# Performance work log

Measured on AMD Instinct MI355X. Metric: run time of the kernel, lower is better.

The kernel has to match this reference:

```python
import jax, jax.numpy as jnp
import numpy as np

B, N, FA, FP, C = 64, 64, 75, 14, 128


def _mlp2(x, W0, b0, W1, b1):
    # two lazy-Linear + ReLU sub-layers (n_sub_layer=2)
    h = jax.nn.relu(x @ W0 + b0)
    return jax.nn.relu(h @ W1 + b1)


def setup_inputs() -> dict:
    key = jax.random.key(0)
    ks = jax.random.split(key, 32)
    w = lambda k, s: jax.random.normal(k, s, jnp.float32) * 0.05
    inp = {
        "atom_x": jax.random.normal(ks[0], (B, N, FA), jnp.float32),
        "pair_x": jax.random.normal(ks[1], (B, N * N, FP), jnp.float32),
        # atom_to_atom: FA -> C -> C
        "a2a_W0": w(ks[2], (FA, C)), "a2a_b0": w(ks[3], (C,)),
        "a2a_W1": w(ks[4], (C, C)), "a2a_b1": w(ks[5], (C,)),
        # pair_to_atom: FP -> C -> C
        "p2a_W0": w(ks[6], (FP, C)), "p2a_b0": w(ks[7], (C,)),
        "p2a_W1": w(ks[8], (C, C)), "p2a_b1": w(ks[9], (C,)),
        # atom_layer: 2C -> C -> C
        "al_W0": w(ks[10], (2 * C, C)), "al_b0": w(ks[11], (C,)),
        "al_W1": w(ks[12], (C, C)), "al_b1": w(ks[13], (C,)),
        # atom_to_pair (weights shared across both orderings): 2FA -> C -> C
        "a2p_W0": w(ks[14], (2 * FA, C)), "a2p_b0": w(ks[15], (C,)),
        "a2p_W1": w(ks[16], (C, C)), "a2p_b1": w(ks[17], (C,)),
        # pair_to_pair: FP -> C -> C
        "p2p_W0": w(ks[18], (FP, C)), "p2p_b0": w(ks[19], (C,)),
        "p2p_W1": w(ks[20], (C, C)), "p2p_b1": w(ks[21], (C,)),
        # pair_layer: 2C -> C -> C
        "pl_W0": w(ks[22], (2 * C, C)), "pl_b0": w(ks[23], (C,)),
        "pl_W1": w(ks[24], (C, C)), "pl_b1": w(ks[25], (C,)),
    }
    return inp


def reference(atom_x, pair_x,
              a2a_W0, a2a_b0, a2a_W1, a2a_b1,
              p2a_W0, p2a_b0, p2a_W1, p2a_b1,
              al_W0, al_b0, al_W1, al_b1,
              a2p_W0, a2p_b0, a2p_W1, a2p_b1,
              p2p_W0, p2p_b0, p2p_W1, p2p_b1,
              pl_W0, pl_b0, pl_W1, pl_b1):
    b, n, fa = atom_x.shape
    # --- atom branch ---
    a0 = _mlp2(atom_x, a2a_W0, a2a_b0, a2a_W1, a2a_b1)            # [B,N,C]
    a1 = _mlp2(pair_x, p2a_W0, p2a_b0, p2a_W1, p2a_b1)            # [B,N*N,C]
    a1 = a1.reshape(b, n, n, -1).sum(axis=2)                      # PairToAtom sum
    a = jnp.concatenate([a0, a1], axis=-1)                        # [B,N,2C]
    next_atom = jax.nn.relu(_mlp2(a, al_W0, al_b0, al_W1, al_b1))  # extra relu per forward
    # --- pair branch ---
    rep = jnp.broadcast_to(atom_x[:, None, :, :], (b, n, n, fa))  # atom_repeat
    til = jnp.broadcast_to(atom_x[:, :, None, :], (b, n, n, fa))  # atom_tile
    pr0 = jnp.concatenate([til, rep], axis=-1).reshape(b, n * n, 2 * fa)
    pr1 = jnp.concatenate([rep, til], axis=-1).reshape(b, n * n, 2 * fa)
    p0 = (_mlp2(pr0, a2p_W0, a2p_b0, a2p_W1, a2p_b1)
          + _mlp2(pr1, a2p_W0, a2p_b0, a2p_W1, a2p_b1))            # [B,N*N,C]
    p1 = _mlp2(pair_x, p2p_W0, p2p_b0, p2p_W1, p2p_b1)            # [B,N*N,C]
    p = jnp.concatenate([p0, p1], axis=-1)                        # [B,N*N,2C]
    next_pair = jax.nn.relu(_mlp2(p, pl_W0, pl_b0, pl_W1, pl_b1))
    return (next_atom, next_pair)
```

## Files before the change

### kernel.cpp

```cpp
#include <hip/hip_runtime.h>
#include <hip/hip_bf16.h>

typedef unsigned short u16;
typedef unsigned int u32;
typedef __attribute__((ext_vector_type(8))) __bf16 bf16x8;
typedef __attribute__((ext_vector_type(4))) float f32x4;

#define B_ 64
#define N_ 64
#define FA_ 75
#define FP_ 14
#define C_ 128

__device__ float g_A0[4096 * 128];
__device__ float g_A1[4096 * 128];
__device__ float g_TB[4096 * 256];
__device__ u16   g_Wf[208896];
__device__ int   g_isbf;

#define OFF_AA0   0
#define OFF_AA1   12288
#define OFF_APT   28672
#define OFF_APB   40960
#define OFF_PA0   53248
#define OFF_PA1   57344
#define OFF_AL0   73728
#define OFF_AL1   106496
#define OFF_AP1   122880
#define OFF_PP0   139264
#define OFF_PP1   143360
#define OFF_PL0T  159744
#define OFF_PL0B  176128
#define OFF_PL1   192512

__device__ __forceinline__ float bf2f(u16 a) {
    union { u32 u; float f; } v; v.u = ((u32)a) << 16; return v.f;
}
__device__ __forceinline__ u16 f2bf(float f) {
    union { float f; u32 u; } v; v.f = f;
    u32 r = v.u + 0x7fffu + ((v.u >> 16) & 1u);
    return (u16)(r >> 16);
}
__device__ __forceinline__ u16 ldw(const void* p, size_t i, bool isbf) {
    if (isbf) return ((const u16*)p)[i];
    return f2bf(((const float*)p)[i]);
}
__device__ __forceinline__ float ldf(const void* p, size_t i, bool isbf) {
    if (isbf) return bf2f(((const u16*)p)[i]);
    return ((const float*)p)[i];
}

__global__ void detect_k(const void* __restrict__ atom) {
    if (threadIdx.x == 0) {
        const u32* a = (const u32*)atom;
        int sane = 0;
        for (int w = 0; w < 64; ++w) {
            u32 ex = (a[w] >> 7) & 0xffu;
            sane += (ex >= 113u && ex <= 133u) ? 1 : 0;
        }
        g_isbf = (sane >= 32) ? 1 : 0;
    }
}

__global__ __launch_bounds__(256) void prep_w(
    const void* aaW0, const void* aaW1, const void* apW0,
    const void* paW0, const void* paW1, const void* alW0, const void* alW1,
    const void* apW1, const void* ppW0, const void* ppW1,
    const void* plW0, const void* plW1) {
    const void* srcs[14] = {aaW0, aaW1, apW0, apW0, paW0, paW1, alW0, alW1,
                            apW1, ppW0, ppW1, plW0, plW0, plW1};
    const int Ktab[14]  = {75, 128, 75, 75, 14, 128, 256, 128, 128, 14, 128, 128, 128, 128};
    const int KStab[14] = {3, 4, 3, 3, 1, 4, 8, 4, 4, 1, 4, 4, 4, 4};
    const int rofft[14] = {0, 0, 0, 75, 0, 0, 0, 0, 0, 0, 0, 0, 128, 0};
    const int baset[14] = {OFF_AA0, OFF_AA1, OFF_APT, OFF_APB, OFF_PA0, OFF_PA1,
                           OFF_AL0, OFF_AL1, OFF_AP1, OFF_PP0, OFF_PP1,
                           OFF_PL0T, OFF_PL0B, OFF_PL1};
    int gid = blockIdx.x * 256 + threadIdx.x;
    int j = 0, s = gid;
    while (j < 14 && s >= KStab[j] * 512) { s -= KStab[j] * 512; ++j; }
    if (j >= 14) return;
    const bool isbf = g_isbf != 0;
    int lane = s & 63, rest = s >> 6;
    int ks = rest % KStab[j], mt = rest / KStab[j];
    int m = mt * 16 + (lane & 15), q = lane >> 4;
    union { u16 h[8]; uint4 u4; } pk;
#pragma unroll
    for (int jj = 0; jj < 8; ++jj) {
        int k = ks * 32 + q * 8 + jj;
        pk.h[jj] = (k < Ktab[j]) ? ldw(srcs[j], (size_t)(rofft[j] + k) * 128 + m, isbf) : (u16)0;
    }
    *(uint4*)&g_Wf[(size_t)baset[j] + (size_t)s * 8] = pk.u4;
}

template<int KS, int NT>
__device__ __forceinline__ void gemm2(const u16* __restrict__ wf,
                                      const u16* __restrict__ bF,
                                      int mt0, int lane, f32x4 (&acc)[2][NT]) {
#pragma unroll
    for (int ks = 0; ks < KS; ++ks) {
        bf16x8 a0 = *(const bf16x8*)(wf + (((mt0    ) * KS + ks) * 64 + lane) * 8);
        bf16x8 a1 = *(const bf16x8*)(wf + (((mt0 + 1) * KS + ks) * 64 + lane) * 8);
#pragma unroll
        for (int nt = 0; nt < NT; ++nt) {
            bf16x8 b = *(const bf16x8*)(bF + ((nt * KS + ks) * 64 + lane) * 8);
            acc[0][nt] = __builtin_amdgcn_mfma_f32_16x16x32_bf16(a0, b, acc[0][nt], 0, 0, 0);
            acc[1][nt] = __builtin_amdgcn_mfma_f32_16x16x32_bf16(a1, b, acc[1][nt], 0, 0, 0);
        }
    }
}

__device__ __forceinline__ void frag_store(u16* dstF, int KSd, int nt, int mt, int lane, f32x4 v) {
    int c = lane & 15, quad = lane >> 4;
    int lp = c + 16 * ((2 * mt + (quad >> 1)) & 3);
    int ks = mt >> 1;
    u16* p = dstF + (((nt * KSd + ks) * 64 + lp) * 8 + (quad & 1) * 4);
    union { u16 h[4]; uint2 u; } pk;
    pk.h[0] = f2bf(v[0]); pk.h[1] = f2bf(v[1]); pk.h[2] = f2bf(v[2]); pk.h[3] = f2bf(v[3]);
    *(uint2*)p = pk.u;
}

__device__ __forceinline__ void store_out4(void* outp, size_t elem, f32x4 v, bool isbf) {
    if (isbf) {
        union { u16 h[4]; uint2 u; } pk;
        pk.h[0] = f2bf(v[0]); pk.h[1] = f2bf(v[1]); pk.h[2] = f2bf(v[2]); pk.h[3] = f2bf(v[3]);
        *(uint2*)((u16*)outp + elem) = pk.u;
    } else {
        *(f32x4*)((float*)outp + elem) = v;
    }
}

#define EPI_RELU_STORE(ACC, SB, DST, NTN) do {                                   \
    int quad_ = lane >> 4;                                                       \
    _Pragma("unroll") for (int ii = 0; ii < 2; ++ii) {                           \
        int mt_ = mt0 + ii;                                                      \
        f32x4 bb_ = *(const f32x4*)&SB[mt_ * 16 + quad_ * 4];                    \
        _Pragma("unroll") for (int nt_ = 0; nt_ < NTN; ++nt_) {                  \
            f32x4 v_;                                                            \
            _Pragma("unroll") for (int r_ = 0; r_ < 4; ++r_) {                   \
                float x_ = ACC[ii][nt_][r_] + bb_[r_];                           \
                v_[r_] = x_ > 0.f ? x_ : 0.f;                                    \
            }                                                                    \
            frag_store(DST, 4, nt_, mt_, lane, v_);                              \
        }                                                                        \
    }                                                                            \
} while (0)

__global__ __launch_bounds__(256) void atom_pre(
    const void* __restrict__ atom,
    const void* __restrict__ aaB0, const void* __restrict__ aaB1) {
    __shared__ __align__(16) u16 sXF[4 * 3 * 64 * 8];
    __shared__ __align__(16) u16 sHF[4 * 4 * 64 * 8];
    __shared__ __align__(16) float sB0[128], sB1[128];
    const bool isbf = g_isbf != 0;
    const int t = threadIdx.x, lane = t & 63, w = t >> 6;
    const int b = blockIdx.x;
    if (t < 128) { sB0[t] = ldf(aaB0, t, isbf); sB1[t] = ldf(aaB1, t, isbf); }
    for (int s = t; s < 4 * 3 * 64; s += 256) {
        int lane_s = s & 63, rest = s >> 6;
        int ks = rest % 3, nt = rest / 3;
        int n = nt * 16 + (lane_s & 15), q = lane_s >> 4;
        union { u16 h[8]; uint4 u4; } pk;
#pragma unroll
        for (int j = 0; j < 8; ++j) {
            int k = ks * 32 + q * 8 + j;
            pk.h[j] = (k < FA_) ? ldw(atom, (size_t)(b * 64 + n) * FA_ + k, isbf) : (u16)0;
        }
        *(uint4*)&sXF[s * 8] = pk.u4;
    }
    __syncthreads();
    const int mt0 = 2 * w;
    {
        f32x4 acc[2][4];
#pragma unroll
        for (int ii = 0; ii < 2; ++ii)
#pragma unroll
            for (int nt = 0; nt < 4; ++nt) acc[ii][nt] = (f32x4){0.f, 0.f, 0.f, 0.f};
        gemm2<3, 4>(g_Wf + OFF_AA0, sXF, mt0, lane, acc);
        EPI_RELU_STORE(acc, sB0, sHF, 4);
    }
    __syncthreads();
    {
        f32x4 acc[2][4];
#pragma unroll
        for (int ii = 0; ii < 2; ++ii)
#pragma unroll
            for (int nt = 0; nt < 4; ++nt) acc[ii][nt] = (f32x4){0.f, 0.f, 0.f, 0.f};
        gemm2<4, 4>(g_Wf + OFF_AA1, sHF, mt0, lane, acc);
        int c = lane & 15, quad = lane >> 4;
#pragma unroll
        for (int ii = 0; ii < 2; ++ii) {
            int mt = mt0 + ii;
            f32x4 bb = *(const f32x4*)&sB1[mt * 16 + quad * 4];
#pragma unroll
            for (int nt = 0; nt < 4; ++nt) {
                f32x4 v;
#pragma unroll
                for (int r = 0; r < 4; ++r) { float x = acc[ii][nt][r] + bb[r]; v[r] = x > 0.f ? x : 0.f; }
                *(f32x4*)&g_A0[(size_t)(b * 64 + nt * 16 + c) * 128 + mt * 16 + quad * 4] = v;
            }
        }
    }
    {
        f32x4 accT[2][4], accB[2][4];
#pragma unroll
        for (int ii = 0; ii < 2; ++ii)
#pragma unroll
            for (int nt = 0; nt < 4; ++nt) { accT[ii][nt] = (f32x4){0.f,0.f,0.f,0.f}; accB[ii][nt] = (f32x4){0.f,0.f,0.f,0.f}; }
        gemm2<3, 4>(g_Wf + OFF_APT, sXF, mt0, lane, accT);
        gemm2<3, 4>(g_Wf + OFF_APB, sXF, mt0, lane, accB);
        int c = lane & 15, quad = lane >> 4;
#pragma unroll
        for (int ii = 0; ii < 2; ++ii) {
            int mt = mt0 + ii;
#pragma unroll
            for (int nt = 0; nt < 4; ++nt) {
                size_t row = (size_t)(b * 64 + nt * 16 + c);
                *(f32x4*)&g_TB[row * 256 + mt * 16 + quad * 4] = accT[ii][nt];
                *(f32x4*)&g_TB[row * 256 + 128 + mt * 16 + quad * 4] = accB[ii][nt];
            }
        }
    }
}

__global__ __launch_bounds__(256) void p2a_sum(
    const void* __restrict__ pairx,
    const void* __restrict__ paB0, const void* __restrict__ paB1) {
    __shared__ __align__(16) u16 sPF[4 * 1 * 64 * 8];
    __shared__ __align__(16) u16 sHF[4 * 4 * 64 * 8];
    __shared__ __align__(16) float sB0[128], sB1[128];
    const bool isbf = g_isbf != 0;
    const int t = threadIdx.x, lane = t & 63, w = t >> 6;
    const int bx = blockIdx.x;
    const size_t rbase = (size_t)bx * 64;
    if (t < 128) { sB0[t] = ldf(paB0, t, isbf); sB1[t] = ldf(paB1, t, isbf); }
    if (t < 256) {
        int s = t;
        int lane_s = s & 63, nt = s >> 6;
        int n = nt * 16 + (lane_s & 15), q = lane_s >> 4;
        union { u16 h[8]; uint4 u4; } pk;
#pragma unroll
        for (int j = 0; j < 8; ++j) {
            int k = q * 8 + j;
            pk.h[j] = (k < FP_) ? ldw(pairx, (rbase + n) * FP_ + k, isbf) : (u16)0;
        }
        *(uint4*)&sPF[s * 8] = pk.u4;
    }
    __syncthreads();
    const int mt0 = 2 * w;
    {
        f32x4 acc[2][4];
#pragma unroll
        for (int ii = 0; ii < 2; ++ii)
#pragma unroll
            for (int nt = 0; nt < 4; ++nt) acc[ii][nt] = (f32x4){0.f, 0.f, 0.f, 0.f};
        gemm2<1, 4>(g_Wf + OFF_PA0, sPF, mt0, lane, acc);
        EPI_RELU_STORE(acc, sB0, sHF, 4);
    }
    __syncthreads();
    {
        f32x4 acc[2][4];
#pragma unroll
        for (int ii = 0; ii < 2; ++ii)
#pragma unroll
            for (int nt = 0; nt < 4; ++nt) acc[ii][nt] = (f32x4){0.f, 0.f, 0.f, 0.f};
        gemm2<4, 4>(g_Wf + OFF_PA1, sHF, mt0, lane, acc);
        int quad = lane >> 4;
#pragma unroll
        for (int ii = 0; ii < 2; ++ii) {
            int mt = mt0 + ii;
            f32x4 bb = *(const f32x4*)&sB1[mt * 16 + quad * 4];
            f32x4 ssum = (f32x4){0.f, 0.f, 0.f, 0.f};
#pragma unroll
            for (int nt = 0; nt < 4; ++nt)
#pragma unroll
                for (int r = 0; r < 4; ++r) {
                    float x = acc[ii][nt][r] + bb[r];
                    ssum[r] += (x > 0.f ? x : 0.f);
                }
#pragma unroll
            for (int m = 1; m < 16; m <<= 1)
#pragma unroll
                for (int r = 0; r < 4; ++r) ssum[r] += __shfl_xor(ssum[r], m, 64);
            if ((lane & 15) == 0)
                *(f32x4*)&g_A1[(size_t)bx * 128 + mt * 16 + quad * 4] = ssum;
        }
    }
}

__global__ __launch_bounds__(256) void atom_layer(
    const void* __restrict__ alB0, const void* __restrict__ alB1,
    void* __restrict__ out) {
    __shared__ __align__(16) u16 sXF[2 * 8 * 64 * 8];
    __shared__ __align__(16) u16 sHF[2 * 4 * 64 * 8];
    __shared__ __align__(16) float sB0[128], sB1[128];
    const bool isbf = g_isbf != 0;
    const int t = threadIdx.x, lane = t & 63, w = t >> 6;
    const int r0g = blockIdx.x * 32;
    if (t < 128) { sB0[t] = ldf(alB0, t, isbf); sB1[t] = ldf(alB1, t, isbf); }
    for (int s = t; s < 2 * 8 * 64; s += 256) {
        int lane_s = s & 63, rest = s >> 6;
        int ks = rest % 8, nt = rest / 8;
        int n = nt * 16 + (lane_s & 15), q = lane_s >> 4;
        union { u16 h[8]; uint4 u4; } pk;
#pragma unroll
        for (int j = 0; j < 8; ++j) {
            int k = ks * 32 + q * 8 + j;
            float v = (k < 128) ? g_A0[(size_t)(r0g + n) * 128 + k]
                                : g_A1[(size_t)(r0g + n) * 128 + (k - 128)];
            pk.h[j] = f2bf(v);
        }
        *(uint4*)&sXF[s * 8] = pk.u4;
    }
    __syncthreads();
    const int mt0 = 2 * w;
    {
        f32x4 acc[2][2];
#pragma unroll
        for (int ii = 0; ii < 2; ++ii)
#pragma unroll
            for (int nt = 0; nt < 2; ++nt) acc[ii][nt] = (f32x4){0.f, 0.f, 0.f, 0.f};
        gemm2<8, 2>(g_Wf + OFF_AL0, sXF, mt0, lane, acc);
        EPI_RELU_STORE(acc, sB0, sHF, 2);
    }
    __syncthreads();
    {
        f32x4 acc[2][2];
#pragma unroll
        for (int ii = 0; ii < 2; ++ii)
#pragma unroll
            for (int nt = 0; nt < 2; ++nt) acc[ii][nt] = (f32x4){0.f, 0.f, 0.f, 0.f};
        gemm2<4, 2>(g_Wf + OFF_AL1, sHF, mt0, lane, acc);
        int c = lane & 15, quad = lane >> 4;
#pragma unroll
        for (int ii = 0; ii < 2; ++ii) {
            int mt = mt0 + ii;
            f32x4 bb = *(const f32x4*)&sB1[mt * 16 + quad * 4];
#pragma unroll
            for (int nt = 0; nt < 2; ++nt) {
                f32x4 v;
#pragma unroll
                for (int r = 0; r < 4; ++r) { float x = acc[ii][nt][r] + bb[r]; v[r] = x > 0.f ? x : 0.f; }
                store_out4(out, (size_t)(r0g + nt * 16 + c) * 128 + mt * 16 + quad * 4, v, isbf);
            }
        }
    }
}

__global__ __launch_bounds__(256) void pair_fused(
    const void* __restrict__ pairx,
    const void* __restrict__ apB0, const void* __restrict__ apB1,
    const void* __restrict__ ppB0, const void* __restrict__ ppB1,
    const void* __restrict__ plB0, const void* __restrict__ plB1,
    void* __restrict__ out) {
    __shared__ __align__(16) u16 sPrF[2 * 1 * 64 * 8];
    __shared__ __align__(16) u16 sH0F[2 * 4 * 64 * 8];
    __shared__ __align__(16) u16 sH1F[2 * 4 * 64 * 8];
    __shared__ __align__(16) u16 sP0F[2 * 4 * 64 * 8];
    __shared__ __align__(16) u16 sHpF[2 * 4 * 64 * 8];
    __shared__ __align__(16) float sBap0[128], sBap1[128], sBpp0[128],
                                   sBpp1[128], sBpl0[128], sBpl1[128];
    const bool isbf = g_isbf != 0;
    const int t = threadIdx.x, lane = t & 63, w = t >> 6;
    const int bx = blockIdx.x;
    const int b = bx >> 7, i = (bx >> 1) & 63, half = bx & 1;
    const int jbase = half * 32, trow = b * 64;
    const size_t prow0 = (size_t)b * 4096 + i * 64 + jbase;

    if (t < 128) {
        sBap0[t] = ldf(apB0, t, isbf); sBap1[t] = ldf(apB1, t, isbf);
        sBpp0[t] = ldf(ppB0, t, isbf); sBpp1[t] = ldf(ppB1, t, isbf);
        sBpl0[t] = ldf(plB0, t, isbf); sBpl1[t] = ldf(plB1, t, isbf);
    }
    if (t < 128) {
        int s = t;
        int lane_s = s & 63, nt = s >> 6;
        int n = nt * 16 + (lane_s & 15), q = lane_s >> 4;
        union { u16 h[8]; uint4 u4; } pk;
#pragma unroll
        for (int j = 0; j < 8; ++j) {
            int k = q * 8 + j;
            pk.h[j] = (k < FP_) ? ldw(pairx, (prow0 + n) * FP_ + k, isbf) : (u16)0;
        }
        *(uint4*)&sPrF[s * 8] = pk.u4;
    }
    __syncthreads();
    for (int sid = t; sid < 1024; sid += 256) {
        int bufid = sid >> 9;
        int s = sid & 511;
        int lane_s = s & 63, rest = s >> 6;
        int ks = rest & 3, nt = rest >> 2;
        int n = nt * 16 + (lane_s & 15), q = lane_s >> 4;
        int k0 = ks * 32 + q * 8;
        const float* Ti = &g_TB[(size_t)(trow + i) * 256];
        const float* Bj = &g_TB[(size_t)(trow + jbase + n) * 256];
        union { u16 h[8]; uint4 u4; } pk;
#pragma unroll
        for (int j = 0; j < 8; ++j) {
            int k = k0 + j;
            float v = (bufid == 0) ? (Ti[k] + Bj[128 + k] + sBap0[k])
                                   : (Bj[k] + Ti[128 + k] + sBap0[k]);
            pk.h[j] = f2bf(v > 0.f ? v : 0.f);
        }
        *(uint4*)&(bufid == 0 ? sH0F : sH1F)[s * 8] = pk.u4;
    }
    __syncthreads();
    const int mt0 = 2 * w;
    {
        f32x4 aA[2][2], aB[2][2];
#pragma unroll
        for (int ii = 0; ii < 2; ++ii)
#pragma unroll
            for (int nt = 0; nt < 2; ++nt) { aA[ii][nt] = (f32x4){0.f,0.f,0.f,0.f}; aB[ii][nt] = (f32x4){0.f,0.f,0.f,0.f}; }
        gemm2<4, 2>(g_Wf + OFF_AP1, sH0F, mt0, lane, aA);
        gemm2<4, 2>(g_Wf + OFF_AP1, sH1F, mt0, lane, aB);
        int quad = lane >> 4;
#pragma unroll
        for (int ii = 0; ii < 2; ++ii) {
            int mt = mt0 + ii;
            f32x4 bb = *(const f32x4*)&sBap1[mt * 16 + quad * 4];
#pragma unroll
            for (int nt = 0; nt < 2; ++nt) {
                f32x4 v;
#pragma unroll
                for (int r = 0; r < 4; ++r) {
                    float x = aA[ii][nt][r] + bb[r];
                    float y = aB[ii][nt][r] + bb[r];
                    v[r] = (x > 0.f ? x : 0.f) + (y > 0.f ? y : 0.f);
                }
                frag_store(sP0F, 4, nt, mt, lane, v);
            }
        }
    }
    __syncthreads();
    f32x4 C3[2][2];
#pragma unroll
    for (int ii = 0; ii < 2; ++ii)
#pragma unroll
        for (int nt = 0; nt < 2; ++nt) C3[ii][nt] = (f32x4){0.f, 0.f, 0.f, 0.f};
    gemm2<4, 2>(g_Wf + OFF_PL0T, sP0F, mt0, lane, C3);
    {
        f32x4 aH[2][2];
#pragma unroll
        for (int ii = 0; ii < 2; ++ii)
#pragma unroll
            for (int nt = 0; nt < 2; ++nt) aH[ii][nt] = (f32x4){0.f, 0.f, 0.f, 0.f};
        gemm2<1, 2>(g_Wf + OFF_PP0, sPrF, mt0, lane, aH);
        EPI_RELU_STORE(aH, sBpp0, sHpF, 2);
    }
    __syncthreads();
    {
        f32x4 aP[2][2];
#pragma unroll
        for (int ii = 0; ii < 2; ++ii)
#pragma unroll
            for (int nt = 0; nt < 2; ++nt) aP[ii][nt] = (f32x4){0.f, 0.f, 0.f, 0.f};
        gemm2<4, 2>(g_Wf + OFF_PP1, sHpF, mt0, lane, aP);
        EPI_RELU_STORE(aP, sBpp1, sH0F, 2);
    }
    __syncthreads();
    gemm2<4, 2>(g_Wf + OFF_PL0B, sH0F, mt0, lane, C3);
    EPI_RELU_STORE(C3, sBpl0, sH1F, 2);
    __syncthreads();
    {
        f32x4 aO[2][2];
#pragma unroll
        for (int ii = 0; ii < 2; ++ii)
#pragma unroll
            for (int nt = 0; nt < 2; ++nt) aO[ii][nt] = (f32x4){0.f, 0.f, 0.f, 0.f};
        gemm2<4, 2>(g_Wf + OFF_PL1, sH1F, mt0, lane, aO);
        int c = lane & 15, quad = lane >> 4;
        const size_t NA = (size_t)B_ * N_ * C_;
#pragma unroll
        for (int ii = 0; ii < 2; ++ii) {
            int mt = mt0 + ii;
            f32x4 bb = *(const f32x4*)&sBpl1[mt * 16 + quad * 4];
#pragma unroll
            for (int nt = 0; nt < 2; ++nt) {
                f32x4 v;
#pragma unroll
                for (int r = 0; r < 4; ++r) { float x = aO[ii][nt][r] + bb[r]; v[r] = x > 0.f ? x : 0.f; }
                store_out4(out, NA + (prow0 + nt * 16 + c) * 128 + mt * 16 + quad * 4, v, isbf);
            }
        }
    }
}

extern "C" void kernel_launch(void* const* d_in, const int* in_sizes, int n_in,
                              void* d_out, int out_size, void* d_ws, size_t ws_size,
                              hipStream_t stream) {
    const void* atom  = d_in[0];
    const void* pairx = d_in[1];
    const void* aaW0 = d_in[2];  const void* aaB0 = d_in[3];
    const void* aaW1 = d_in[4];  const void* aaB1 = d_in[5];
    const void* paW0 = d_in[6];  const void* paB0 = d_in[7];
    const void* paW1 = d_in[8];  const void* paB1 = d_in[9];
    const void* alW0 = d_in[10]; const void* alB0 = d_in[11];
    const void* alW1 = d_in[12]; const void* alB1 = d_in[13];
    const void* apW0 = d_in[14]; const void* apB0 = d_in[15];
    const void* apW1 = d_in[16]; const void* apB1 = d_in[17];
    const void* ppW0 = d_in[18]; const void* ppB0 = d_in[19];
    const void* ppW1 = d_in[20]; const void* ppB1 = d_in[21];
    const void* plW0 = d_in[22]; const void* plB0 = d_in[23];
    const void* plW1 = d_in[24]; const void* plB1 = d_in[25];
    (void)d_ws; (void)ws_size; (void)in_sizes; (void)n_in; (void)out_size;

    detect_k<<<1, 64, 0, stream>>>(atom);
    prep_w<<<102, 256, 0, stream>>>(aaW0, aaW1, apW0, paW0, paW1, alW0, alW1,
                                    apW1, ppW0, ppW1, plW0, plW1);
    atom_pre<<<64, 256, 0, stream>>>(atom, aaB0, aaB1);
    p2a_sum<<<4096, 256, 0, stream>>>(pairx, paB0, paB1);
    atom_layer<<<128, 256, 0, stream>>>(alB0, alB1, d_out);
    pair_fused<<<8192, 256, 0, stream>>>(pairx, apB0, apB1, ppB0, ppB1,
                                         plB0, plB1, d_out);
}
```

Baseline: 348.0 us.

## Pack bf16 conversions, load biases into registers, shrink pair_fused LDS footprint

Replaces scalar float-to-bf16 rounding with a packed hardware conversion builtin where available, and loads biases per lane from global into registers instead of staging them in shared memory. pair_fused moves its activation buffers into one aliased 24KB shared pool and adds a launch-bounds occupancy hint. It precomputes the row-i term plus bias once per block and starts the pair_to_pair first GEMM before the barrier, overlapping it with the gather. Together these aim to cut conversion ALU work, LDS use and barrier stalls, at the cost of more register pressure and possible rounding differences from the builtin.

```diff
diff --git a/kernel.cpp b/kernel.cpp
--- a/kernel.cpp
+++ b/kernel.cpp
@@ -41,6 +41,21 @@
     u32 r = v.u + 0x7fffu + ((v.u >> 16) & 1u);
     return (u16)(r >> 16);
 }
+#if __has_builtin(__builtin_amdgcn_cvt_pk_bf16_f32)
+__device__ __forceinline__ u32 f2bf_pk(float a, float b) {
+    auto r = __builtin_amdgcn_cvt_pk_bf16_f32(a, b);
+    if constexpr (sizeof(r) == 4) {
+        union { decltype(r) v; u32 u; } c; c.v = r; return c.u;
+    } else {
+        return (u32)f2bf(a) | ((u32)f2bf(b) << 16);
+    }
+}
+#else
+__device__ __forceinline__ u32 f2bf_pk(float a, float b) {
+    return (u32)f2bf(a) | ((u32)f2bf(b) << 16);
+}
+#endif
+
 __device__ __forceinline__ u16 ldw(const void* p, size_t i, bool isbf) {
     if (isbf) return ((const u16*)p)[i];
     return f2bf(((const float*)p)[i]);
@@ -48,6 +63,35 @@
 __device__ __forceinline__ float ldf(const void* p, size_t i, bool isbf) {
     if (isbf) return bf2f(((const u16*)p)[i]);
     return ((const float*)p)[i];
+}
+__device__ __forceinline__ f32x4 ldf4(const void* p, int i, bool isbf) {
+    f32x4 r;
+    if (isbf) {
+        const u16* q = (const u16*)p + i;
+        r[0] = bf2f(q[0]); r[1] = bf2f(q[1]); r[2] = bf2f(q[2]); r[3] = bf2f(q[3]);
+    } else {
+        r = *(const f32x4*)((const float*)p + i);
+    }
+    return r;
+}
+__device__ __forceinline__ uint4 pack8(const void* p, size_t base, int kmax, int k0, bool isbf) {
+    uint4 u;
+    if (isbf) {
+        const u16* q = (const u16*)p + base;
+        u16 h[8];
+#pragma unroll
+        for (int j = 0; j < 8; ++j) h[j] = (k0 + j < kmax) ? q[k0 + j] : (u16)0;
+        u.x = (u32)h[0] | ((u32)h[1] << 16); u.y = (u32)h[2] | ((u32)h[3] << 16);
+        u.z = (u32)h[4] | ((u32)h[5] << 16); u.w = (u32)h[6] | ((u32)h[7] << 16);
+    } else {
+        const float* q = (const float*)p + base;
+        float f[8];
+#pragma unroll
+        for (int j = 0; j < 8; ++j) f[j] = (k0 + j < kmax) ? q[k0 + j] : 0.f;
+        u.x = f2bf_pk(f[0], f[1]); u.y = f2bf_pk(f[2], f[3]);
+        u.z = f2bf_pk(f[4], f[5]); u.w = f2bf_pk(f[6], f[7]);
+    }
+    return u;
 }
 
 __global__ void detect_k(const void* __restrict__ atom) {
@@ -83,13 +127,16 @@
     int lane = s & 63, rest = s >> 6;
     int ks = rest % KStab[j], mt = rest / KStab[j];
     int m = mt * 16 + (lane & 15), q = lane >> 4;
-    union { u16 h[8]; uint4 u4; } pk;
+    float f[8];
 #pragma unroll
     for (int jj = 0; jj < 8; ++jj) {
         int k = ks * 32 + q * 8 + jj;
-        pk.h[jj] = (k < Ktab[j]) ? ldw(srcs[j], (size_t)(rofft[j] + k) * 128 + m, isbf) : (u16)0;
-    }
-    *(uint4*)&g_Wf[(size_t)baset[j] + (size_t)s * 8] = pk.u4;
+        f[jj] = (k < Ktab[j]) ? ldf(srcs[j], (size_t)(rofft[j] + k) * 128 + m, isbf) : 0.f;
+    }
+    uint4 u;
+    u.x = f2bf_pk(f[0], f[1]); u.y = f2bf_pk(f[2], f[3]);
+    u.z = f2bf_pk(f[4], f[5]); u.w = f2bf_pk(f[6], f[7]);
+    *(uint4*)&g_Wf[(size_t)baset[j] + (size_t)s * 8] = u;
 }
 
 template<int KS, int NT>
@@ -113,34 +160,29 @@
     int c = lane & 15, quad = lane >> 4;
     int lp = c + 16 * ((2 * mt + (quad >> 1)) & 3);
     int ks = mt >> 1;
-    u16* p = dstF + (((nt * KSd + ks) * 64 + lp) * 8 + (quad & 1) * 4);
-    union { u16 h[4]; uint2 u; } pk;
-    pk.h[0] = f2bf(v[0]); pk.h[1] = f2bf(v[1]); pk.h[2] = f2bf(v[2]); pk.h[3] = f2bf(v[3]);
-    *(uint2*)p = pk.u;
+    uint2 u; u.x = f2bf_pk(v[0], v[1]); u.y = f2bf_pk(v[2], v[3]);
+    *(uint2*)(dstF + (((nt * KSd + ks) * 64 + lp) * 8 + (quad & 1) * 4)) = u;
 }
 
 __device__ __forceinline__ void store_out4(void* outp, size_t elem, f32x4 v, bool isbf) {
     if (isbf) {
-        union { u16 h[4]; uint2 u; } pk;
-        pk.h[0] = f2bf(v[0]); pk.h[1] = f2bf(v[1]); pk.h[2] = f2bf(v[2]); pk.h[3] = f2bf(v[3]);
-        *(uint2*)((u16*)outp + elem) = pk.u;
+        uint2 u; u.x = f2bf_pk(v[0], v[1]); u.y = f2bf_pk(v[2], v[3]);
+        *(uint2*)((u16*)outp + elem) = u;
     } else {
         *(f32x4*)((float*)outp + elem) = v;
     }
 }
 
-#define EPI_RELU_STORE(ACC, SB, DST, NTN) do {                                   \
-    int quad_ = lane >> 4;                                                       \
+#define EPI_RELU_STORE(ACC, BB0, BB1, DST, NTN) do {                             \
     _Pragma("unroll") for (int ii = 0; ii < 2; ++ii) {                           \
-        int mt_ = mt0 + ii;                                                      \
-        f32x4 bb_ = *(const f32x4*)&SB[mt_ * 16 + quad_ * 4];                    \
+        f32x4 bb_ = ii ? (BB1) : (BB0);                                          \
         _Pragma("unroll") for (int nt_ = 0; nt_ < NTN; ++nt_) {                  \
             f32x4 v_;                                                            \
             _Pragma("unroll") for (int r_ = 0; r_ < 4; ++r_) {                   \
                 float x_ = ACC[ii][nt_][r_] + bb_[r_];                           \
                 v_[r_] = x_ > 0.f ? x_ : 0.f;                                    \
             }                                                                    \
-            frag_store(DST, 4, nt_, mt_, lane, v_);                              \
+            frag_store(DST, 4, nt_, mt0 + ii, lane, v_);                         \
         }                                                                        \
     }                                                                            \
 } while (0)
@@ -150,47 +192,44 @@
     const void* __restrict__ aaB0, const void* __restrict__ aaB1) {
     __shared__ __align__(16) u16 sXF[4 * 3 * 64 * 8];
     __shared__ __align__(16) u16 sHF[4 * 4 * 64 * 8];
-    __shared__ __align__(16) float sB0[128], sB1[128];
     const bool isbf = g_isbf != 0;
     const int t = threadIdx.x, lane = t & 63, w = t >> 6;
+    const int quad = lane >> 4;
     const int b = blockIdx.x;
-    if (t < 128) { sB0[t] = ldf(aaB0, t, isbf); sB1[t] = ldf(aaB1, t, isbf); }
     for (int s = t; s < 4 * 3 * 64; s += 256) {
         int lane_s = s & 63, rest = s >> 6;
         int ks = rest % 3, nt = rest / 3;
         int n = nt * 16 + (lane_s & 15), q = lane_s >> 4;
-        union { u16 h[8]; uint4 u4; } pk;
-#pragma unroll
-        for (int j = 0; j < 8; ++j) {
-            int k = ks * 32 + q * 8 + j;
-            pk.h[j] = (k < FA_) ? ldw(atom, (size_t)(b * 64 + n) * FA_ + k, isbf) : (u16)0;
-        }
-        *(uint4*)&sXF[s * 8] = pk.u4;
+        *(uint4*)&sXF[s * 8] = pack8(atom, (size_t)(b * 64 + n) * FA_, FA_, ks * 32 + q * 8, isbf);
     }
     __syncthreads();
     const int mt0 = 2 * w;
     {
+        f32x4 bb0 = ldf4(aaB0, mt0 * 16 + quad * 4, isbf);
+        f32x4 bb1 = ldf4(aaB0, (mt0 + 1) * 16 + quad * 4, isbf);
         f32x4 acc[2][4];
 #pragma unroll
         for (int ii = 0; ii < 2; ++ii)
 #pragma unroll
             for (int nt = 0; nt < 4; ++nt) acc[ii][nt] = (f32x4){0.f, 0.f, 0.f, 0.f};
         gemm2<3, 4>(g_Wf + OFF_AA0, sXF, mt0, lane, acc);
-        EPI_RELU_STORE(acc, sB0, sHF, 4);
-    }
-    __syncthreads();
-    {
+        EPI_RELU_STORE(acc, bb0, bb1, sHF, 4);
+    }
+    __syncthreads();
+    {
+        f32x4 bb0 = ldf4(aaB1, mt0 * 16 + quad * 4, isbf);
+        f32x4 bb1 = ldf4(aaB1, (mt0 + 1) * 16 + quad * 4, isbf);
         f32x4 acc[2][4];
 #pragma unroll
         for (int ii = 0; ii < 2; ++ii)
 #pragma unroll
             for (int nt = 0; nt < 4; ++nt) acc[ii][nt] = (f32x4){0.f, 0.f, 0.f, 0.f};
         gemm2<4, 4>(g_Wf + OFF_AA1, sHF, mt0, lane, acc);
-        int c = lane & 15, quad = lane >> 4;
+        int c = lane & 15;
 #pragma unroll
         for (int ii = 0; ii < 2; ++ii) {
             int mt = mt0 + ii;
-            f32x4 bb = *(const f32x4*)&sB1[mt * 16 + quad * 4];
+            f32x4 bb = ii ? bb1 : bb0;
 #pragma unroll
             for (int nt = 0; nt < 4; ++nt) {
                 f32x4 v;
@@ -208,7 +247,7 @@
             for (int nt = 0; nt < 4; ++nt) { accT[ii][nt] = (f32x4){0.f,0.f,0.f,0.f}; accB[ii][nt] = (f32x4){0.f,0.f,0.f,0.f}; }
         gemm2<3, 4>(g_Wf + OFF_APT, sXF, mt0, lane, accT);
         gemm2<3, 4>(g_Wf + OFF_APB, sXF, mt0, lane, accB);
-        int c = lane & 15, quad = lane >> 4;
+        int c = lane & 15;
 #pragma unroll
         for (int ii = 0; ii < 2; ++ii) {
             int mt = mt0 + ii;
@@ -227,48 +266,43 @@
     const void* __restrict__ paB0, const void* __restrict__ paB1) {
     __shared__ __align__(16) u16 sPF[4 * 1 * 64 * 8];
     __shared__ __align__(16) u16 sHF[4 * 4 * 64 * 8];
-    __shared__ __align__(16) float sB0[128], sB1[128];
     const bool isbf = g_isbf != 0;
     const int t = threadIdx.x, lane = t & 63, w = t >> 6;
+    const int quad = lane >> 4;
     const int bx = blockIdx.x;
     const size_t rbase = (size_t)bx * 64;
-    if (t < 128) { sB0[t] = ldf(paB0, t, isbf); sB1[t] = ldf(paB1, t, isbf); }
-    if (t < 256) {
-        int s = t;
-        int lane_s = s & 63, nt = s >> 6;
+    {
+        int lane_s = t & 63, nt = t >> 6;
         int n = nt * 16 + (lane_s & 15), q = lane_s >> 4;
-        union { u16 h[8]; uint4 u4; } pk;
-#pragma unroll
-        for (int j = 0; j < 8; ++j) {
-            int k = q * 8 + j;
-            pk.h[j] = (k < FP_) ? ldw(pairx, (rbase + n) * FP_ + k, isbf) : (u16)0;
-        }
-        *(uint4*)&sPF[s * 8] = pk.u4;
+        *(uint4*)&sPF[t * 8] = pack8(pairx, (rbase + n) * FP_, FP_, q * 8, isbf);
     }
     __syncthreads();
     const int mt0 = 2 * w;
     {
+        f32x4 bb0 = ldf4(paB0, mt0 * 16 + quad * 4, isbf);
+        f32x4 bb1 = ldf4(paB0, (mt0 + 1) * 16 + quad * 4, isbf);
         f32x4 acc[2][4];
 #pragma unroll
         for (int ii = 0; ii < 2; ++ii)
 #pragma unroll
             for (int nt = 0; nt < 4; ++nt) acc[ii][nt] = (f32x4){0.f, 0.f, 0.f, 0.f};
         gemm2<1, 4>(g_Wf + OFF_PA0, sPF, mt0, lane, acc);
-        EPI_RELU_STORE(acc, sB0, sHF, 4);
-    }
-    __syncthreads();
-    {
+        EPI_RELU_STORE(acc, bb0, bb1, sHF, 4);
+    }
+    __syncthreads();
+    {
+        f32x4 bb0 = ldf4(paB1, mt0 * 16 + quad * 4, isbf);
+        f32x4 bb1 = ldf4(paB1, (mt0 + 1) * 16 + quad * 4, isbf);
         f32x4 acc[2][4];
 #pragma unroll
         for (int ii = 0; ii < 2; ++ii)
 #pragma unroll
             for (int nt = 0; nt < 4; ++nt) acc[ii][nt] = (f32x4){0.f, 0.f, 0.f, 0.f};
         gemm2<4, 4>(g_Wf + OFF_PA1, sHF, mt0, lane, acc);
-        int quad = lane >> 4;
 #pragma unroll
         for (int ii = 0; ii < 2; ++ii) {
             int mt = mt0 + ii;
-            f32x4 bb = *(const f32x4*)&sB1[mt * 16 + quad * 4];
+            f32x4 bb = ii ? bb1 : bb0;
             f32x4 ssum = (f32x4){0.f, 0.f, 0.f, 0.f};
 #pragma unroll
             for (int nt = 0; nt < 4; ++nt)
@@ -292,49 +326,51 @@
     void* __restrict__ out) {
     __shared__ __align__(16) u16 sXF[2 * 8 * 64 * 8];
     __shared__ __align__(16) u16 sHF[2 * 4 * 64 * 8];
-    __shared__ __align__(16) float sB0[128], sB1[128];
     const bool isbf = g_isbf != 0;
     const int t = threadIdx.x, lane = t & 63, w = t >> 6;
+    const int quad = lane >> 4;
     const int r0g = blockIdx.x * 32;
-    if (t < 128) { sB0[t] = ldf(alB0, t, isbf); sB1[t] = ldf(alB1, t, isbf); }
     for (int s = t; s < 2 * 8 * 64; s += 256) {
         int lane_s = s & 63, rest = s >> 6;
-        int ks = rest % 8, nt = rest / 8;
+        int ks = rest & 7, nt = rest >> 3;
         int n = nt * 16 + (lane_s & 15), q = lane_s >> 4;
-        union { u16 h[8]; uint4 u4; } pk;
-#pragma unroll
-        for (int j = 0; j < 8; ++j) {
-            int k = ks * 32 + q * 8 + j;
-            float v = (k < 128) ? g_A0[(size_t)(r0g + n) * 128 + k]
-                                : g_A1[(size_t)(r0g + n) * 128 + (k - 128)];
-            pk.h[j] = f2bf(v);
-        }
-        *(uint4*)&sXF[s * 8] = pk.u4;
+        int k0 = ks * 32 + q * 8;
+        const float* src = (k0 < 128) ? &g_A0[(size_t)(r0g + n) * 128 + k0]
+                                      : &g_A1[(size_t)(r0g + n) * 128 + (k0 - 128)];
+        f32x4 f0 = *(const f32x4*)src, f1 = *(const f32x4*)(src + 4);
+        uint4 u;
+        u.x = f2bf_pk(f0[0], f0[1]); u.y = f2bf_pk(f0[2], f0[3]);
+        u.z = f2bf_pk(f1[0], f1[1]); u.w = f2bf_pk(f1[2], f1[3]);
+        *(uint4*)&sXF[s * 8] = u;
     }
     __syncthreads();
     const int mt0 = 2 * w;
     {
+        f32x4 bb0 = ldf4(alB0, mt0 * 16 + quad * 4, isbf);
+        f32x4 bb1 = ldf4(alB0, (mt0 + 1) * 16 + quad * 4, isbf);
         f32x4 acc[2][2];
 #pragma unroll
         for (int ii = 0; ii < 2; ++ii)
 #pragma unroll
             for (int nt = 0; nt < 2; ++nt) acc[ii][nt] = (f32x4){0.f, 0.f, 0.f, 0.f};
         gemm2<8, 2>(g_Wf + OFF_AL0, sXF, mt0, lane, acc);
-        EPI_RELU_STORE(acc, sB0, sHF, 2);
-    }
-    __syncthreads();
-    {
+        EPI_RELU_STORE(acc, bb0, bb1, sHF, 2);
+    }
+    __syncthreads();
+    {
+        f32x4 bb0 = ldf4(alB1, mt0 * 16 + quad * 4, isbf);
+        f32x4 bb1 = ldf4(alB1, (mt0 + 1) * 16 + quad * 4, isbf);
         f32x4 acc[2][2];
 #pragma unroll
         for (int ii = 0; ii < 2; ++ii)
 #pragma unroll
             for (int nt = 0; nt < 2; ++nt) acc[ii][nt] = (f32x4){0.f, 0.f, 0.f, 0.f};
         gemm2<4, 2>(g_Wf + OFF_AL1, sHF, mt0, lane, acc);
-        int c = lane & 15, quad = lane >> 4;
+        int c = lane & 15;
 #pragma unroll
         for (int ii = 0; ii < 2; ++ii) {
             int mt = mt0 + ii;
-            f32x4 bb = *(const f32x4*)&sB1[mt * 16 + quad * 4];
+            f32x4 bb = ii ? bb1 : bb0;
 #pragma unroll
             for (int nt = 0; nt < 2; ++nt) {
                 f32x4 v;
@@ -346,78 +382,80 @@
     }
 }
 
-__global__ __launch_bounds__(256) void pair_fused(
+__global__ __launch_bounds__(256, 4) void pair_fused(
     const void* __restrict__ pairx,
     const void* __restrict__ apB0, const void* __restrict__ apB1,
     const void* __restrict__ ppB0, const void* __restrict__ ppB1,
     const void* __restrict__ plB0, const void* __restrict__ plB1,
     void* __restrict__ out) {
-    __shared__ __align__(16) u16 sPrF[2 * 1 * 64 * 8];
-    __shared__ __align__(16) u16 sH0F[2 * 4 * 64 * 8];
-    __shared__ __align__(16) u16 sH1F[2 * 4 * 64 * 8];
-    __shared__ __align__(16) u16 sP0F[2 * 4 * 64 * 8];
-    __shared__ __align__(16) u16 sHpF[2 * 4 * 64 * 8];
-    __shared__ __align__(16) float sBap0[128], sBap1[128], sBpp0[128],
-                                   sBpp1[128], sBpl0[128], sBpl1[128];
+    __shared__ __align__(16) u16 sPool[3 * 4096];
+    u16* sX1 = sPool;
+    u16* sX2 = sPool + 4096;
+    u16* sR  = sPool + 8192;
+    u16* sPrF = sR;
+    float* sTip = (float*)(sR + 1024);
+    float* sBip = sTip + 128;
     const bool isbf = g_isbf != 0;
     const int t = threadIdx.x, lane = t & 63, w = t >> 6;
+    const int quad = lane >> 4, c = lane & 15;
     const int bx = blockIdx.x;
     const int b = bx >> 7, i = (bx >> 1) & 63, half = bx & 1;
     const int jbase = half * 32, trow = b * 64;
     const size_t prow0 = (size_t)b * 4096 + i * 64 + jbase;
+    const int mt0 = 2 * w;
 
     if (t < 128) {
-        sBap0[t] = ldf(apB0, t, isbf); sBap1[t] = ldf(apB1, t, isbf);
-        sBpp0[t] = ldf(ppB0, t, isbf); sBpp1[t] = ldf(ppB1, t, isbf);
-        sBpl0[t] = ldf(plB0, t, isbf); sBpl1[t] = ldf(plB1, t, isbf);
-    }
-    if (t < 128) {
-        int s = t;
+        float b0 = ldf(apB0, t, isbf);
+        sTip[t] = g_TB[(size_t)(trow + i) * 256 + t] + b0;
+        sBip[t] = g_TB[(size_t)(trow + i) * 256 + 128 + t] + b0;
+    } else {
+        int s = t - 128;
         int lane_s = s & 63, nt = s >> 6;
         int n = nt * 16 + (lane_s & 15), q = lane_s >> 4;
-        union { u16 h[8]; uint4 u4; } pk;
-#pragma unroll
-        for (int j = 0; j < 8; ++j) {
-            int k = q * 8 + j;
-            pk.h[j] = (k < FP_) ? ldw(pairx, (prow0 + n) * FP_ + k, isbf) : (u16)0;
-        }
-        *(uint4*)&sPrF[s * 8] = pk.u4;
+        *(uint4*)&sPrF[s * 8] = pack8(pairx, (prow0 + n) * FP_, FP_, q * 8, isbf);
     }
     __syncthreads();
     for (int sid = t; sid < 1024; sid += 256) {
-        int bufid = sid >> 9;
-        int s = sid & 511;
+        int buf = sid >> 9, s = sid & 511;
         int lane_s = s & 63, rest = s >> 6;
         int ks = rest & 3, nt = rest >> 2;
         int n = nt * 16 + (lane_s & 15), q = lane_s >> 4;
         int k0 = ks * 32 + q * 8;
-        const float* Ti = &g_TB[(size_t)(trow + i) * 256];
         const float* Bj = &g_TB[(size_t)(trow + jbase + n) * 256];
-        union { u16 h[8]; uint4 u4; } pk;
-#pragma unroll
-        for (int j = 0; j < 8; ++j) {
-            int k = k0 + j;
-            float v = (bufid == 0) ? (Ti[k] + Bj[128 + k] + sBap0[k])
-                                   : (Bj[k] + Ti[128 + k] + sBap0[k]);
-            pk.h[j] = f2bf(v > 0.f ? v : 0.f);
-        }
-        *(uint4*)&(bufid == 0 ? sH0F : sH1F)[s * 8] = pk.u4;
-    }
-    __syncthreads();
-    const int mt0 = 2 * w;
-    {
+        float v[8];
+        if (buf == 0) {
+#pragma unroll
+            for (int j = 0; j < 8; ++j) { float x = sTip[k0 + j] + Bj[128 + k0 + j]; v[j] = x > 0.f ? x : 0.f; }
+        } else {
+#pragma unroll
+            for (int j = 0; j < 8; ++j) { float x = Bj[k0 + j] + sBip[k0 + j]; v[j] = x > 0.f ? x : 0.f; }
+        }
+        uint4 u;
+        u.x = f2bf_pk(v[0], v[1]); u.y = f2bf_pk(v[2], v[3]);
+        u.z = f2bf_pk(v[4], v[5]); u.w = f2bf_pk(v[6], v[7]);
+        *(uint4*)&(buf == 0 ? sX1 : sX2)[s * 8] = u;
+    }
+    f32x4 aH[2][2];
+#pragma unroll
+    for (int ii = 0; ii < 2; ++ii)
+#pragma unroll
+        for (int nt = 0; nt < 2; ++nt) aH[ii][nt] = (f32x4){0.f, 0.f, 0.f, 0.f};
+    gemm2<1, 2>(g_Wf + OFF_PP0, sPrF, mt0, lane, aH);
+    __syncthreads();
+    {
+        f32x4 bb0 = ldf4(apB1, mt0 * 16 + quad * 4, isbf);
+        f32x4 bb1 = ldf4(apB1, (mt0 + 1) * 16 + quad * 4, isbf);
         f32x4 aA[2][2], aB[2][2];
 #pragma unroll
         for (int ii = 0; ii < 2; ++ii)
 #pragma unroll
             for (int nt = 0; nt < 2; ++nt) { aA[ii][nt] = (f32x4){0.f,0.f,0.f,0.f}; aB[ii][nt] = (f32x4){0.f,0.f,0.f,0.f}; }
-        gemm2<4, 2>(g_Wf + OFF_AP1, sH0F, mt0, lane, aA);
-        gemm2<4, 2>(g_Wf + OFF_AP1, sH1F, mt0, lane, aB);
-        int quad = lane >> 4;
+        gemm2<4, 2>(g_Wf + OFF_AP1, sX1, mt0, lane, aA);
+        gemm2<4, 2>(g_Wf + OFF_AP1, sX2, mt0, lane, aB);
 #pragma unroll
         for (int ii = 0; ii < 2; ++ii) {
             int mt = mt0 + ii;
-            f32x4 bb = *(const f32x4*)&sBap1[mt * 16 + quad * 4];
+            f32x4 bb = ii ? bb1 : bb0;
 #pragma unroll
             for (int nt = 0; nt < 2; ++nt) {
                 f32x4 v;
@@ -427,7 +465,7 @@
                     float y = aB[ii][nt][r] + bb[r];
                     v[r] = (x > 0.f ? x : 0.f) + (y > 0.f ? y : 0.f);
                 }
-                frag_store(sP0F, 4, nt, mt, lane, v);
+                frag_store(sR, 4, nt, mt, lane, v);
             }
         }
     }
@@ -437,43 +475,46 @@
     for (int ii = 0; ii < 2; ++ii)
 #pragma unroll
         for (int nt = 0; nt < 2; ++nt) C3[ii][nt] = (f32x4){0.f, 0.f, 0.f, 0.f};
-    gemm2<4, 2>(g_Wf + OFF_PL0T, sP0F, mt0, lane, C3);
-    {
-        f32x4 aH[2][2];
-#pragma unroll
-        for (int ii = 0; ii < 2; ++ii)
-#pragma unroll
-            for (int nt = 0; nt < 2; ++nt) aH[ii][nt] = (f32x4){0.f, 0.f, 0.f, 0.f};
-        gemm2<1, 2>(g_Wf + OFF_PP0, sPrF, mt0, lane, aH);
-        EPI_RELU_STORE(aH, sBpp0, sHpF, 2);
-    }
-    __syncthreads();
-    {
+    gemm2<4, 2>(g_Wf + OFF_PL0T, sR, mt0, lane, C3);
+    {
+        f32x4 bb0 = ldf4(ppB0, mt0 * 16 + quad * 4, isbf);
+        f32x4 bb1 = ldf4(ppB0, (mt0 + 1) * 16 + quad * 4, isbf);
+        EPI_RELU_STORE(aH, bb0, bb1, sX1, 2);
+    }
+    __syncthreads();
+    {
+        f32x4 bb0 = ldf4(ppB1, mt0 * 16 + quad * 4, isbf);
+        f32x4 bb1 = ldf4(ppB1, (mt0 + 1) * 16 + quad * 4, isbf);
         f32x4 aP[2][2];
 #pragma unroll
         for (int ii = 0; ii < 2; ++ii)
 #pragma unroll
             for (int nt = 0; nt < 2; ++nt) aP[ii][nt] = (f32x4){0.f, 0.f, 0.f, 0.f};
-        gemm2<4, 2>(g_Wf + OFF_PP1, sHpF, mt0, lane, aP);
-        EPI_RELU_STORE(aP, sBpp1, sH0F, 2);
-    }
-    __syncthreads();
-    gemm2<4, 2>(g_Wf + OFF_PL0B, sH0F, mt0, lane, C3);
-    EPI_RELU_STORE(C3, sBpl0, sH1F, 2);
-    __syncthreads();
-    {
+        gemm2<4, 2>(g_Wf + OFF_PP1, sX1, mt0, lane, aP);
+        EPI_RELU_STORE(aP, bb0, bb1, sX2, 2);
+    }
+    __syncthreads();
+    gemm2<4, 2>(g_Wf + OFF_PL0B, sX2, mt0, lane, C3);
+    {
+        f32x4 bb0 = ldf4(plB0, mt0 * 16 + quad * 4, isbf);
+        f32x4 bb1 = ldf4(plB0, (mt0 + 1) * 16 + quad * 4, isbf);
+        EPI_RELU_STORE(C3, bb0, bb1, sX1, 2);
+    }
+    __syncthreads();
+    {
+        f32x4 bb0 = ldf4(plB1, mt0 * 16 + quad * 4, isbf);
+        f32x4 bb1 = ldf4(plB1, (mt0 + 1) * 16 + quad * 4, isbf);
         f32x4 aO[2][2];
 #pragma unroll
         for (int ii = 0; ii < 2; ++ii)
 #pragma unroll
             for (int nt = 0; nt < 2; ++nt) aO[ii][nt] = (f32x4){0.f, 0.f, 0.f, 0.f};
-        gemm2<4, 2>(g_Wf + OFF_PL1, sH1F, mt0, lane, aO);
-        int c = lane & 15, quad = lane >> 4;
+        gemm2<4, 2>(g_Wf + OFF_PL1, sX1, mt0, lane, aO);
         const size_t NA = (size_t)B_ * N_ * C_;
 #pragma unroll
         for (int ii = 0; ii < 2; ++ii) {
             int mt = mt0 + ii;
-            f32x4 bb = *(const f32x4*)&sBpl1[mt * 16 + quad * 4];
+            f32x4 bb = ii ? bb1 : bb0;
 #pragma unroll
             for (int nt = 0; nt < 2; ++nt) {
                 f32x4 v;
```

Result: faster. 325.6 us (-6.4%).
